# Optimization experiments

Hardware: AMD Instinct MI355X
Metric: run time of the kernel (lower is better)

## Reference

```python
import jax, jax.numpy as jnp
import numpy as np

# Config (matches init_kwargs)
B, C, H, W = 32, 128, 12, 1200   # z: (B, in_dim, H, W)
DIN = C * H                       # 1536
FIX = 768                         # get_multiple(DIN // 2, 6)
OV = 4                            # overlap
G = 6                             # num_vqs
D = OV * FIX // G                 # 512 per-group embedding size (all equal)
K = 1024                          # codebook_size
COMMIT = 0.25


def setup_inputs() -> dict:
    key = jax.random.key(0)
    k1, k2, k3, k4 = jax.random.split(key, 4)
    z = jax.random.normal(k1, (B, C, H, W), dtype=jnp.float32)
    w_down = jax.random.normal(k2, (FIX, DIN), dtype=jnp.float32) * 0.02
    w_up = jax.random.normal(k3, (DIN, FIX), dtype=jnp.float32) * 0.02
    embedding = jax.random.normal(k4, (G, D, K), dtype=jnp.float32)  # per-group (embedding_size, num_embedding)
    return {"z": z, "w_down": w_down, "w_up": w_up, "embedding": embedding}


def _quantize_group(zg, emb):
    # zg: (B, T, D), emb: (D, K)
    zf = zg.reshape(-1, D)
    # squared euclidean distance: |z|^2 - 2 z@E + |E|^2 -> (N, K)
    dist = (zf * zf).sum(1, keepdims=True) - 2.0 * (zf @ emb) + (emb * emb).sum(0, keepdims=True)
    idx = jnp.argmin(dist, axis=1)            # (N,)
    q = jnp.take(emb.T, idx, axis=0).reshape(zg.shape)
    # straight-through estimator (training mode)
    zq = zg + jax.lax.stop_gradient(q - zg)
    loss = COMMIT * jnp.mean((jax.lax.stop_gradient(zq) - zg) ** 2)
    return zq, loss


def reference(z, w_down, w_up, embedding):
    # pre_process: (B,C,H,W) -> permute(0,2,3,1) -> permute(0,2,3,1) -> (B, W, C*H)
    x = jnp.transpose(z, (0, 3, 1, 2)).reshape(B, W, DIN)  # (B, W, C, H) flattened
    x = x @ w_down.T                                       # proj_down -> (B, W, FIX)
    T = W // OV
    x = x.reshape(B, T, OV * FIX)                          # (B, T, 3072)
    # split into G contiguous groups of size D along last axis -> (G, B, T, D)
    xg = jnp.transpose(x.reshape(B, T, G, D), (2, 0, 1, 3))
    zq_g, losses = jax.vmap(_quantize_group)(xg, embedding)
    vq_loss = losses.sum() / G
    # concat groups back -> (B, T, G*D)
    zq = jnp.transpose(zq_g, (1, 2, 0, 3)).reshape(B, T, G * D)
    # post_process: un-overlap, proj_up, back to (B, C, H, W)
    zq = zq.reshape(B, W, FIX)
    zq = zq @ w_up.T                                       # (B, W, DIN)
    zq = zq.reshape(B, W, C, H)
    zq = jnp.transpose(zq, (0, 3, 1, 2))                   # (B, H, W, C)
    zq = jnp.transpose(zq, (0, 3, 1, 2))                   # dim==4 -> (B, C, H, W)
    return zq, vq_loss
```

## Files before the change

### kernel.cpp

```cpp
#include <hip/hip_runtime.h>

#define BB 32
#define CC 128
#define HH 12
#define WW 1200
#define DIN 1536
#define FIXD 768
#define OVL 4
#define GG 6
#define DD 512
#define KK 1024
#define TT 300
#define NV 9600
#define MROWS 38400

#define Y_OFF     0
#define ET_OFF    29491200
#define NORM_OFF  32636928
#define BEST_OFF  32643072
#define LOSS_OFF  32758272
#define ZN_OFF    32758336

#define BSWZ(c) ((c) + 4 * ((c) >> 5))

__global__ __launch_bounds__(256) void k_gemm_down(const float* __restrict__ z,
                                                   const float* __restrict__ w_down,
                                                   float* __restrict__ Y) {
    __shared__ float As[16][132];
    __shared__ float Bs[16][140];
    const int n0 = blockIdx.y * 128, f0 = blockIdx.x * 128;
    const int tid = threadIdx.x;
    const int arow = tid & 127;
    const int ak0 = tid >> 7;
    const int nA = n0 + arow;
    const int bA = nA / WW, wA = nA - bA * WW;
    const size_t zbase = (size_t)bA * (CC * HH * WW) + wA;
    const int bcol = tid >> 1, bq = tid & 1;
    const int bsc = BSWZ(bcol);
    const int trow = tid >> 4, tcol = tid & 15;
    const int bread = tcol * 8 + 4 * (tcol >> 2);
    float acc[8][8] = {};
    for (int kt = 0; kt < DIN; kt += 16) {
        #pragma unroll
        for (int i = 0; i < 8; i++) {
            const int kk = ak0 + i * 2;
            As[kk][arow] = z[zbase + (size_t)(kt + kk) * WW];
        }
        #pragma unroll
        for (int i = 0; i < 2; i++) {
            const int q = bq + i * 2;
            const float4 v = *(const float4*)&w_down[(size_t)(f0 + bcol) * DIN + kt + q * 4];
            Bs[q * 4 + 0][bsc] = v.x;
            Bs[q * 4 + 1][bsc] = v.y;
            Bs[q * 4 + 2][bsc] = v.z;
            Bs[q * 4 + 3][bsc] = v.w;
        }
        __syncthreads();
        #pragma unroll
        for (int k = 0; k < 16; k++) {
            float av[8], bv[8];
            *(float4*)&av[0] = *(const float4*)&As[k][trow * 8];
            *(float4*)&av[4] = *(const float4*)&As[k][trow * 8 + 4];
            *(float4*)&bv[0] = *(const float4*)&Bs[k][bread];
            *(float4*)&bv[4] = *(const float4*)&Bs[k][bread + 4];
            #pragma unroll
            for (int i = 0; i < 8; i++)
                #pragma unroll
                for (int j = 0; j < 8; j++)
                    acc[i][j] = fmaf(av[i], bv[j], acc[i][j]);
        }
        __syncthreads();
    }
    #pragma unroll
    for (int i = 0; i < 8; i++) {
        float4 o0, o1;
        o0.x = acc[i][0]; o0.y = acc[i][1]; o0.z = acc[i][2]; o0.w = acc[i][3];
        o1.x = acc[i][4]; o1.y = acc[i][5]; o1.z = acc[i][6]; o1.w = acc[i][7];
        float* yr = &Y[(size_t)(n0 + trow * 8 + i) * FIXD + f0 + tcol * 8];
        *(float4*)yr = o0;
        *(float4*)(yr + 4) = o1;
    }
}

__global__ __launch_bounds__(256) void k_transpose(const float* __restrict__ emb,
                                                   float* __restrict__ ET) {
    int i = blockIdx.x * 256 + threadIdx.x;
    if (i >= GG * KK * DD) return;
    int d = i & 511;
    int rem = i >> 9;
    int k = rem & 1023;
    int g = rem >> 10;
    ET[i] = emb[((g * DD + d) << 10) + k];
}

__global__ __launch_bounds__(64) void k_norms(const float* __restrict__ ET,
                                              float* __restrict__ norms) {
    const int code = blockIdx.x;
    const int lane = threadIdx.x;
    const float* row = ET + code * DD;
    double s = 0.0;
    #pragma unroll
    for (int r = 0; r < 8; r++) {
        float v = row[lane + r * 64];
        s += (double)v * (double)v;
    }
    #pragma unroll
    for (int off = 32; off; off >>= 1) s += __shfl_down(s, off);
    if (lane == 0) norms[code] = (float)s;
}

__global__ __launch_bounds__(256) void k_dist2(const float* __restrict__ Y,
                                               const float* __restrict__ ET,
                                               const float* __restrict__ norms,
                                               unsigned long long* __restrict__ best,
                                               float* __restrict__ znorm) {
    __shared__ float Zs[16][68];
    __shared__ float Es[16][140];
    __shared__ unsigned long long red[64][17];
    const int r = blockIdx.x;
    const int g = blockIdx.y;
    const int chunk = r / 48;
    const int wi = r - chunk * 48;
    const int vt = chunk * 6 + (wi % 6);
    const int ct = wi / 6;
    const int tid = threadIdx.x;
    const int rgrp = tid >> 4, cgrp = tid & 15;
    const int rbase = rgrp * 4;
    const int eread = cgrp * 8 + 4 * (cgrp >> 2);
    const int v0 = vt * 64, c0 = ct * 128;
    const float* ETg = ET + (size_t)g * KK * DD;

    const int zrow = tid >> 2, zq = tid & 3;
    const int vz = v0 + zrow;
    const int bz = vz / TT, tz = vz - bz * TT;

    float acc[4][8] = {};
    float zs = 0.0f;

    for (int kt = 0; kt < DD; kt += 16) {
        const int p0 = g * DD + kt;
        const int s = p0 / FIXD, f0 = p0 - s * FIXD;
        {
            const float4 v = *(const float4*)&Y[(bz * WW + tz * OVL + s) * FIXD + f0 + zq * 4];
            Zs[zq * 4 + 0][zrow] = v.x;
            Zs[zq * 4 + 1][zrow] = v.y;
            Zs[zq * 4 + 2][zrow] = v.z;
            Zs[zq * 4 + 3][zrow] = v.w;
            if (ct == 0) {
                zs = fmaf(v.x, v.x, zs);
                zs = fmaf(v.y, v.y, zs);
                zs = fmaf(v.z, v.z, zs);
                zs = fmaf(v.w, v.w, zs);
            }
        }
        #pragma unroll
        for (int i = 0; i < 2; i++) {
            int flat = tid + i * 256;
            int code = flat >> 2, q = flat & 3;
            const int sc = BSWZ(code);
            const float4 v = *(const float4*)&ETg[(size_t)(c0 + code) * DD + kt + q * 4];
            Es[q * 4 + 0][sc] = v.x;
            Es[q * 4 + 1][sc] = v.y;
            Es[q * 4 + 2][sc] = v.z;
            Es[q * 4 + 3][sc] = v.w;
        }
        __syncthreads();
        #pragma unroll
        for (int k = 0; k < 16; k++) {
            const float4 z4 = *(const float4*)&Zs[k][rbase];
            const float4 ea = *(const float4*)&Es[k][eread];
            const float4 eb = *(const float4*)&Es[k][eread + 4];
            const float zv[4] = {z4.x, z4.y, z4.z, z4.w};
            const float ev[8] = {ea.x, ea.y, ea.z, ea.w, eb.x, eb.y, eb.z, eb.w};
            #pragma unroll
            for (int i = 0; i < 4; i++)
                #pragma unroll
                for (int j = 0; j < 8; j++)
                    acc[i][j] = fmaf(zv[i], ev[j], acc[i][j]);
        }
        __syncthreads();
    }

    if (ct == 0) {
        float zsum = zs;
        zsum += __shfl_down(zsum, 2);
        zsum += __shfl_down(zsum, 1);
        if (zq == 0) znorm[g * NV + v0 + zrow] = zsum;
    }

    unsigned long long kbest[4];
    #pragma unroll
    for (int i = 0; i < 4; i++) kbest[i] = ~0ull;
    #pragma unroll
    for (int j = 0; j < 8; j++) {
        const int c = c0 + cgrp * 8 + j;
        const float nrm = norms[(g << 10) + c];
        #pragma unroll
        for (int i = 0; i < 4; i++) {
            float score = nrm - 2.0f * acc[i][j];
            unsigned u = __float_as_uint(score);
            u = (u & 0x80000000u) ? ~u : (u | 0x80000000u);
            unsigned long long key = ((unsigned long long)u << 32) | (unsigned)c;
            if (key < kbest[i]) kbest[i] = key;
        }
    }
    #pragma unroll
    for (int i = 0; i < 4; i++) red[rbase + i][cgrp] = kbest[i];
    __syncthreads();
    if (tid < 64) {
        unsigned long long b = red[tid][0];
        #pragma unroll
        for (int j = 1; j < 16; j++) {
            unsigned long long v = red[tid][j];
            if (v < b) b = v;
        }
        atomicMin(&best[g * NV + v0 + tid], b);
    }
}

__global__ __launch_bounds__(256) void k_sumloss(const unsigned long long* __restrict__ best,
                                                 const float* __restrict__ znorm,
                                                 float* __restrict__ lossAcc) {
    const int v = blockIdx.x * 256 + threadIdx.x;
    const unsigned long long key = best[v];
    const unsigned u = (unsigned)(key >> 32);
    const unsigned x = (u & 0x80000000u) ? (u & 0x7fffffffu) : ~u;
    float s = __uint_as_float(x) + znorm[v];
    __shared__ float red[256];
    red[threadIdx.x] = s;
    __syncthreads();
    for (int off = 128; off; off >>= 1) {
        if (threadIdx.x < off) red[threadIdx.x] += red[threadIdx.x + off];
        __syncthreads();
    }
    if (threadIdx.x == 0) atomicAdd(lossAcc, red[0]);
}

__constant__ int SEG_G[8]  = {0, 1, 1, 2, 3, 4, 4, 5};
__constant__ int SEG_D0[8] = {0, 0, 256, 0, 0, 0, 256, 0};
__constant__ int SEG_L[8]  = {512, 256, 256, 512, 512, 256, 256, 512};
__constant__ int SEG_F0[8] = {0, 512, 0, 256, 0, 512, 0, 256};

__global__ __launch_bounds__(256) void k_table(const float* __restrict__ ET,
                                               const float* __restrict__ w_up,
                                               float* __restrict__ Tab) {
    __shared__ float As[16][68];
    __shared__ float Bs[16][140];
    const int bm = blockIdx.x;
    const int bn = blockIdx.y;
    const int seg = blockIdx.z;
    const int g = SEG_G[seg], d0 = SEG_D0[seg], len = SEG_L[seg], fb = SEG_F0[seg];
    const int tid = threadIdx.x;
    const int k0 = bm * 64, dout0 = bn * 128;
    const int arow = tid >> 2, aq = tid & 3;
    const int rbase = (tid >> 4) << 2;
    const int cgrp = tid & 15;
    const int bread = cgrp * 8 + 4 * (cgrp >> 2);
    const float* ETg = ET + (size_t)(g << 10) * DD;
    float acc[4][8] = {};
    for (int kt = 0; kt < len; kt += 16) {
        {
            const float4 v = *(const float4*)&ETg[(size_t)(k0 + arow) * DD + d0 + kt + aq * 4];
            As[aq * 4 + 0][arow] = v.x;
            As[aq * 4 + 1][arow] = v.y;
            As[aq * 4 + 2][arow] = v.z;
            As[aq * 4 + 3][arow] = v.w;
        }
        #pragma unroll
        for (int i = 0; i < 2; i++) {
            int fl = tid + i * 256;
            int col = fl >> 2, q = fl & 3;
            const int sc = BSWZ(col);
            const float4 v = *(const float4*)&w_up[(size_t)(dout0 + col) * FIXD + fb + kt + q * 4];
            Bs[q * 4 + 0][sc] = v.x;
            Bs[q * 4 + 1][sc] = v.y;
            Bs[q * 4 + 2][sc] = v.z;
            Bs[q * 4 + 3][sc] = v.w;
        }
        __syncthreads();
        #pragma unroll
        for (int k = 0; k < 16; k++) {
            const float4 a  = *(const float4*)&As[k][rbase];
            const float4 ba = *(const float4*)&Bs[k][bread];
            const float4 bb = *(const float4*)&Bs[k][bread + 4];
            const float av[4] = {a.x, a.y, a.z, a.w};
            const float bv[8] = {ba.x, ba.y, ba.z, ba.w, bb.x, bb.y, bb.z, bb.w};
            #pragma unroll
            for (int i = 0; i < 4; i++)
                #pragma unroll
                for (int j = 0; j < 8; j++)
                    acc[i][j] = fmaf(av[i], bv[j], acc[i][j]);
        }
        __syncthreads();
    }
    #pragma unroll
    for (int i = 0; i < 4; i++) {
        float4 o0, o1;
        o0.x = acc[i][0]; o0.y = acc[i][1]; o0.z = acc[i][2]; o0.w = acc[i][3];
        o1.x = acc[i][4]; o1.y = acc[i][5]; o1.z = acc[i][6]; o1.w = acc[i][7];
        float* tr = &Tab[(size_t)((seg << 10) + k0 + rbase + i) * DIN + dout0 + cgrp * 8];
        *(float4*)tr = o0;
        *(float4*)(tr + 4) = o1;
    }
}

__global__ __launch_bounds__(256) void k_scatter(const float* __restrict__ Tab,
                                                 const unsigned long long* __restrict__ best,
                                                 float* __restrict__ out) {
    __shared__ float Ls[64][65];
    const int dt = blockIdx.x;
    const int wt = blockIdx.y;
    const int b  = blockIdx.z;
    const int dout0 = dt * 64, w0 = wt * 64;
    const int wlim = (WW - w0 < 64) ? (WW - w0) : 64;
    const int tid = threadIdx.x;
    const int wi = tid >> 2, q = tid & 3;

    if (wi < wlim) {
        const int w = w0 + wi;
        const int s = w & 3;
        const int t = w >> 2;
        const int gEt[4] = {0, 1, 3, 4};
        const int gOt[4] = {1, 2, 4, 5};
        int ce = (int)(unsigned)best[gEt[s] * NV + b * TT + t];
        int co = (int)(unsigned)best[gOt[s] * NV + b * TT + t];
        size_t rowE = (size_t)(((2 * s) << 10) + ce) * DIN;
        size_t rowO = (size_t)(((2 * s + 1) << 10) + co) * DIN;
        #pragma unroll
        for (int rep = 0; rep < 4; rep++) {
            const int doff = rep * 16 + q * 4;
            const float4 a = *(const float4*)&Tab[rowE + dout0 + doff];
            const float4 c = *(const float4*)&Tab[rowO + dout0 + doff];
            Ls[wi][doff + 0] = a.x + c.x;
            Ls[wi][doff + 1] = a.y + c.y;
            Ls[wi][doff + 2] = a.z + c.z;
            Ls[wi][doff + 3] = a.w + c.w;
        }
    }
    __syncthreads();
    const size_t obase = (size_t)b * (CC * HH * WW) + (size_t)dout0 * WW + w0;
    #pragma unroll
    for (int i = 0; i < 16; i++) {
        int flat = tid + i * 256;
        int dr = flat >> 6, wj = flat & 63;
        if (wj < wlim) out[obase + (size_t)dr * WW + wj] = Ls[wj][dr];
    }
}

__global__ void k_finish(const float* __restrict__ lossAcc, float* __restrict__ out) {
    if (threadIdx.x == 0)
        out[58982400] = lossAcc[0] * (0.25f / 29491200.0f);
}

extern "C" void kernel_launch(void* const* d_in, const int* in_sizes, int n_in,
                              void* d_out, int out_size, void* d_ws, size_t ws_size,
                              hipStream_t stream) {
    const float* z      = (const float*)d_in[0];
    const float* w_down = (const float*)d_in[1];
    const float* w_up   = (const float*)d_in[2];
    const float* emb    = (const float*)d_in[3];
    float* out = (float*)d_out;

    float* ws    = (float*)d_ws;
    float* Y     = ws + Y_OFF;
    float* Tab   = ws + Y_OFF;
    float* ET    = ws + ET_OFF;
    float* norms = ws + NORM_OFF;
    unsigned long long* best = (unsigned long long*)(ws + BEST_OFF);
    float* lossA = ws + LOSS_OFF;
    float* znorm = ws + ZN_OFF;

    hipMemsetAsync(best, 0xFF, (size_t)GG * NV * sizeof(unsigned long long), stream);
    hipMemsetAsync(lossA, 0, sizeof(float), stream);

    dim3 gdown(6, 300);
    k_gemm_down<<<gdown, 256, 0, stream>>>(z, w_down, Y);

    k_transpose<<<(GG * KK * DD + 255) / 256, 256, 0, stream>>>(emb, ET);
    k_norms<<<GG * KK, 64, 0, stream>>>(ET, norms);

    dim3 gdist(1200, GG);
    k_dist2<<<gdist, 256, 0, stream>>>(Y, ET, norms, best, znorm);

    k_sumloss<<<225, 256, 0, stream>>>(best, znorm, lossA);

    dim3 gtab(16, 12, 8);
    k_table<<<gtab, 256, 0, stream>>>(ET, w_up, Tab);

    dim3 gsc(24, 19, 32);
    k_scatter<<<gsc, 256, 0, stream>>>(Tab, best, out);

    k_finish<<<1, 64, 0, stream>>>(lossA, out);
}
```

Measured before the change: 2.091 ms.

## Use bf16 MFMA distance pass with candidate filtering and exact fp32 rescoring

Replaces the fp32 FMA distance/argmin kernel with a two-phase bf16 MFMA scheme. The first pass finds an approximate minimum per vector. The second recomputes the distances and collects every code within a Cauchy-Schwarz-based error margin. Those candidates are then rescored exactly in fp32, with a full fallback when more than 64 candidates qualify. This moves the dominant distance GEMM onto matrix cores, but it runs that GEMM twice and adds conversion kernels, atomics and rescoring work, so the argmin only matches the reference as long as the margin covers the bf16 error.

```diff
diff --git a/kernel.cpp b/kernel.cpp
--- a/kernel.cpp
+++ b/kernel.cpp
@@ -20,8 +20,27 @@
 #define BEST_OFF  32643072
 #define LOSS_OFF  32758272
 #define ZN_OFF    32758336
+#define UMIN_OFF  32815936
+#define CNT_OFF   32873536
+#define MAXN_OFF  32931136
+#define LIST_OFF  32931200
+#define YBF_OFF   36617600
+#define EBF_OFF   51363200
 
 #define BSWZ(c) ((c) + 4 * ((c) >> 5))
+
+typedef __attribute__((ext_vector_type(8))) short bf16x8;
+typedef __attribute__((ext_vector_type(4))) float f32x4;
+
+static __device__ inline unsigned short f2bf(float x) {
+    unsigned u = __float_as_uint(x);
+    unsigned r = (u + 0x7fffu + ((u >> 16) & 1u)) >> 16;
+    return (unsigned short)r;
+}
+static __device__ inline unsigned enc32(float s) {
+    unsigned u = __float_as_uint(s);
+    return (u & 0x80000000u) ? ~u : (u | 0x80000000u);
+}
 
 __global__ __launch_bounds__(256) void k_gemm_down(const float* __restrict__ z,
                                                    const float* __restrict__ w_down,
@@ -94,7 +113,8 @@
 }
 
 __global__ __launch_bounds__(64) void k_norms(const float* __restrict__ ET,
-                                              float* __restrict__ norms) {
+                                              float* __restrict__ norms,
+                                              unsigned* __restrict__ maxnU) {
     const int code = blockIdx.x;
     const int lane = threadIdx.x;
     const float* row = ET + code * DD;
@@ -106,116 +126,225 @@
     }
     #pragma unroll
     for (int off = 32; off; off >>= 1) s += __shfl_down(s, off);
-    if (lane == 0) norms[code] = (float)s;
-}
-
-__global__ __launch_bounds__(256) void k_dist2(const float* __restrict__ Y,
-                                               const float* __restrict__ ET,
+    if (lane == 0) {
+        const float nf = (float)s;
+        norms[code] = nf;
+        atomicMax(&maxnU[code >> 10], __float_as_uint(nf));
+    }
+}
+
+__global__ __launch_bounds__(256) void k_ysplit(const float* __restrict__ Y,
+                                                unsigned short* __restrict__ Ybf,
+                                                float* __restrict__ znorm) {
+    const int gv = blockIdx.x * 4 + (threadIdx.x >> 6);
+    const int lane = threadIdx.x & 63;
+    const int g = gv / NV, r = gv - g * NV;
+    const int b = r / TT, t = r - b * TT;
+    const int d0 = lane * 8;
+    const int p = g * DD + d0;
+    const int sg = p / FIXD, f = p - sg * FIXD;
+    const float* yb = &Y[(size_t)((b * WW + t * OVL + sg) * FIXD + f)];
+    const float4 y0 = *(const float4*)yb;
+    const float4 y1 = *(const float4*)(yb + 4);
+    unsigned short h[8];
+    h[0] = f2bf(y0.x); h[1] = f2bf(y0.y); h[2] = f2bf(y0.z); h[3] = f2bf(y0.w);
+    h[4] = f2bf(y1.x); h[5] = f2bf(y1.y); h[6] = f2bf(y1.z); h[7] = f2bf(y1.w);
+    *(uint4*)&Ybf[(size_t)gv * DD + d0] = *(uint4*)&h[0];
+    float s = 0.f;
+    s = fmaf(y0.x, y0.x, s); s = fmaf(y0.y, y0.y, s);
+    s = fmaf(y0.z, y0.z, s); s = fmaf(y0.w, y0.w, s);
+    s = fmaf(y1.x, y1.x, s); s = fmaf(y1.y, y1.y, s);
+    s = fmaf(y1.z, y1.z, s); s = fmaf(y1.w, y1.w, s);
+    #pragma unroll
+    for (int off = 32; off; off >>= 1) s += __shfl_down(s, off);
+    if (lane == 0) znorm[gv] = s;
+}
+
+__global__ __launch_bounds__(256) void k_esplit(const float* __restrict__ ET,
+                                                unsigned short* __restrict__ Ebf) {
+    const size_t i8 = ((size_t)blockIdx.x * 256 + threadIdx.x) * 8;
+    const float4 a = *(const float4*)&ET[i8];
+    const float4 b = *(const float4*)&ET[i8 + 4];
+    unsigned short h[8];
+    h[0] = f2bf(a.x); h[1] = f2bf(a.y); h[2] = f2bf(a.z); h[3] = f2bf(a.w);
+    h[4] = f2bf(b.x); h[5] = f2bf(b.y); h[6] = f2bf(b.z); h[7] = f2bf(b.w);
+    *(uint4*)&Ebf[i8] = *(uint4*)&h[0];
+}
+
+template<int PHASE>
+__global__ __launch_bounds__(256) void k_dist3(const unsigned short* __restrict__ Ybf,
+                                               const unsigned short* __restrict__ Ebf,
                                                const float* __restrict__ norms,
-                                               unsigned long long* __restrict__ best,
-                                               float* __restrict__ znorm) {
-    __shared__ float Zs[16][68];
-    __shared__ float Es[16][140];
-    __shared__ unsigned long long red[64][17];
-    const int r = blockIdx.x;
-    const int g = blockIdx.y;
-    const int chunk = r / 48;
-    const int wi = r - chunk * 48;
-    const int vt = chunk * 6 + (wi % 6);
-    const int ct = wi / 6;
+                                               const float* __restrict__ znorm,
+                                               const unsigned* __restrict__ maxnU,
+                                               unsigned* __restrict__ umin,
+                                               unsigned* __restrict__ cnt,
+                                               unsigned* __restrict__ list_) {
+    __shared__ unsigned short Ah[128][40], Bh[128][40];
+    __shared__ float a1s[128], margs[128];
+    const int vt = blockIdx.x;
+    const int ct = blockIdx.y;
+    const int g  = blockIdx.z;
+    const int v0 = vt * 128, c0 = ct * 128;
     const int tid = threadIdx.x;
-    const int rgrp = tid >> 4, cgrp = tid & 15;
-    const int rbase = rgrp * 4;
-    const int eread = cgrp * 8 + 4 * (cgrp >> 2);
-    const int v0 = vt * 64, c0 = ct * 128;
-    const float* ETg = ET + (size_t)g * KK * DD;
-
-    const int zrow = tid >> 2, zq = tid & 3;
-    const int vz = v0 + zrow;
-    const int bz = vz / TT, tz = vz - bz * TT;
-
-    float acc[4][8] = {};
-    float zs = 0.0f;
-
-    for (int kt = 0; kt < DD; kt += 16) {
-        const int p0 = g * DD + kt;
-        const int s = p0 / FIXD, f0 = p0 - s * FIXD;
+    const size_t ybase = ((size_t)g * NV + v0) * DD;
+    const size_t ebase = ((size_t)g * KK + c0) * DD;
+    const int srow = tid >> 1, sseg = (tid & 1) * 16;
+    const int wv = tid >> 6, lane = tid & 63;
+    const int wr = wv >> 1, wc = wv & 1;
+    const int m0 = wr * 64, n0 = wc * 64;
+    const int lr = lane & 15, lq = lane >> 4;
+
+    if (PHASE == 2 && tid < 128) {
+        const int gv = g * NV + v0 + tid;
+        const unsigned u = umin[gv];
+        const unsigned x = (u & 0x80000000u) ? (u & 0x7fffffffu) : ~u;
+        a1s[tid] = __uint_as_float(x);
+        margs[tid] = 0.032f * sqrtf(znorm[gv] * __uint_as_float(maxnU[g]));
+    }
+
+    f32x4 acc[4][4];
+    #pragma unroll
+    for (int i = 0; i < 4; i++)
+        #pragma unroll
+        for (int j = 0; j < 4; j++) acc[i][j] = (f32x4){0.f, 0.f, 0.f, 0.f};
+
+    for (int kt = 0; kt < DD; kt += 32) {
         {
-            const float4 v = *(const float4*)&Y[(bz * WW + tz * OVL + s) * FIXD + f0 + zq * 4];
-            Zs[zq * 4 + 0][zrow] = v.x;
-            Zs[zq * 4 + 1][zrow] = v.y;
-            Zs[zq * 4 + 2][zrow] = v.z;
-            Zs[zq * 4 + 3][zrow] = v.w;
-            if (ct == 0) {
-                zs = fmaf(v.x, v.x, zs);
-                zs = fmaf(v.y, v.y, zs);
-                zs = fmaf(v.z, v.z, zs);
-                zs = fmaf(v.w, v.w, zs);
+            const uint4 a0 = *(const uint4*)&Ybf[ybase + (size_t)srow * DD + kt + sseg];
+            const uint4 a1 = *(const uint4*)&Ybf[ybase + (size_t)srow * DD + kt + sseg + 8];
+            const uint4 b0 = *(const uint4*)&Ebf[ebase + (size_t)srow * DD + kt + sseg];
+            const uint4 b1 = *(const uint4*)&Ebf[ebase + (size_t)srow * DD + kt + sseg + 8];
+            *(uint4*)&Ah[srow][sseg]     = a0;
+            *(uint4*)&Ah[srow][sseg + 8] = a1;
+            *(uint4*)&Bh[srow][sseg]     = b0;
+            *(uint4*)&Bh[srow][sseg + 8] = b1;
+        }
+        __syncthreads();
+        bf16x8 ah[4], bh[4];
+        #pragma unroll
+        for (int i = 0; i < 4; i++) {
+            ah[i] = *(bf16x8*)&Ah[m0 + i * 16 + lr][lq * 8];
+            bh[i] = *(bf16x8*)&Bh[n0 + i * 16 + lr][lq * 8];
+        }
+        #pragma unroll
+        for (int i = 0; i < 4; i++)
+            #pragma unroll
+            for (int j = 0; j < 4; j++)
+                acc[i][j] = __builtin_amdgcn_mfma_f32_16x16x32_bf16(ah[i], bh[j], acc[i][j], 0, 0, 0);
+        __syncthreads();
+    }
+
+    float nrmj[4];
+    #pragma unroll
+    for (int j = 0; j < 4; j++) nrmj[j] = norms[(g << 10) + c0 + n0 + j * 16 + lr];
+
+    #pragma unroll
+    for (int i = 0; i < 4; i++) {
+        #pragma unroll
+        for (int rr = 0; rr < 4; rr++) {
+            const int row = m0 + i * 16 + lq * 4 + rr;
+            if (PHASE == 1) {
+                unsigned kb = 0xFFFFFFFFu;
+                #pragma unroll
+                for (int j = 0; j < 4; j++) {
+                    const unsigned u = enc32(nrmj[j] - 2.0f * acc[i][j][rr]);
+                    kb = (u < kb) ? u : kb;
+                }
+                #pragma unroll
+                for (int off = 1; off < 16; off <<= 1) {
+                    const unsigned o = __shfl_xor(kb, off);
+                    kb = (o < kb) ? o : kb;
+                }
+                if (lr == 0) atomicMin(&umin[g * NV + v0 + row], kb);
+            } else {
+                const float thr = a1s[row] + margs[row];
+                #pragma unroll
+                for (int j = 0; j < 4; j++) {
+                    const float sc = nrmj[j] - 2.0f * acc[i][j][rr];
+                    if (sc <= thr) {
+                        const int gv = g * NV + v0 + row;
+                        const unsigned idx = atomicAdd(&cnt[gv], 1u);
+                        if (idx < 64u)
+                            list_[(size_t)gv * 64 + idx] = (unsigned)(c0 + n0 + j * 16 + lr);
+                    }
+                }
             }
         }
-        #pragma unroll
-        for (int i = 0; i < 2; i++) {
-            int flat = tid + i * 256;
-            int code = flat >> 2, q = flat & 3;
-            const int sc = BSWZ(code);
-            const float4 v = *(const float4*)&ETg[(size_t)(c0 + code) * DD + kt + q * 4];
-            Es[q * 4 + 0][sc] = v.x;
-            Es[q * 4 + 1][sc] = v.y;
-            Es[q * 4 + 2][sc] = v.z;
-            Es[q * 4 + 3][sc] = v.w;
-        }
-        __syncthreads();
-        #pragma unroll
-        for (int k = 0; k < 16; k++) {
-            const float4 z4 = *(const float4*)&Zs[k][rbase];
-            const float4 ea = *(const float4*)&Es[k][eread];
-            const float4 eb = *(const float4*)&Es[k][eread + 4];
-            const float zv[4] = {z4.x, z4.y, z4.z, z4.w};
-            const float ev[8] = {ea.x, ea.y, ea.z, ea.w, eb.x, eb.y, eb.z, eb.w};
-            #pragma unroll
-            for (int i = 0; i < 4; i++)
-                #pragma unroll
-                for (int j = 0; j < 8; j++)
-                    acc[i][j] = fmaf(zv[i], ev[j], acc[i][j]);
-        }
-        __syncthreads();
-    }
-
-    if (ct == 0) {
-        float zsum = zs;
-        zsum += __shfl_down(zsum, 2);
-        zsum += __shfl_down(zsum, 1);
-        if (zq == 0) znorm[g * NV + v0 + zrow] = zsum;
-    }
-
-    unsigned long long kbest[4];
-    #pragma unroll
-    for (int i = 0; i < 4; i++) kbest[i] = ~0ull;
-    #pragma unroll
-    for (int j = 0; j < 8; j++) {
-        const int c = c0 + cgrp * 8 + j;
-        const float nrm = norms[(g << 10) + c];
-        #pragma unroll
-        for (int i = 0; i < 4; i++) {
-            float score = nrm - 2.0f * acc[i][j];
-            unsigned u = __float_as_uint(score);
-            u = (u & 0x80000000u) ? ~u : (u | 0x80000000u);
-            unsigned long long key = ((unsigned long long)u << 32) | (unsigned)c;
-            if (key < kbest[i]) kbest[i] = key;
-        }
-    }
-    #pragma unroll
-    for (int i = 0; i < 4; i++) red[rbase + i][cgrp] = kbest[i];
+    }
+}
+
+__global__ __launch_bounds__(64) void k_rescore(const float* __restrict__ Y,
+                                                const float* __restrict__ ET,
+                                                const float* __restrict__ norms,
+                                                const unsigned* __restrict__ cnt,
+                                                const unsigned* __restrict__ list_,
+                                                unsigned long long* __restrict__ best) {
+    const int gv = blockIdx.x;
+    const unsigned n = cnt[gv];
+    if (n == 0u || n > 64u) return;
+    const int lane = threadIdx.x;
+    const int g = gv / NV, r = gv - g * NV;
+    const int b = r / TT, t = r - b * TT;
+    unsigned long long key = ~0ull;
+    if (lane < (int)n) {
+        const unsigned c = list_[(size_t)gv * 64 + lane];
+        const float* erow = &ET[((size_t)((g << 10) + c)) * DD];
+        float s = 0.f;
+        for (int d4 = 0; d4 < 128; ++d4) {
+            const int p = g * DD + d4 * 4;
+            const int sg = p / FIXD, f = p - sg * FIXD;
+            const float4 yv = *(const float4*)&Y[(size_t)((b * WW + t * OVL + sg) * FIXD + f)];
+            const float4 ev = *(const float4*)&erow[d4 * 4];
+            s = fmaf(yv.x, ev.x, s); s = fmaf(yv.y, ev.y, s);
+            s = fmaf(yv.z, ev.z, s); s = fmaf(yv.w, ev.w, s);
+        }
+        const float sc = norms[(g << 10) + c] - 2.0f * s;
+        key = ((unsigned long long)enc32(sc) << 32) | c;
+    }
+    #pragma unroll
+    for (int off = 32; off; off >>= 1) {
+        const unsigned long long o = __shfl_down(key, off);
+        if (o < key) key = o;
+    }
+    if (lane == 0) best[gv] = key;
+}
+
+__global__ __launch_bounds__(256) void k_fallback(const float* __restrict__ Y,
+                                                  const float* __restrict__ ET,
+                                                  const float* __restrict__ norms,
+                                                  const unsigned* __restrict__ cnt,
+                                                  unsigned long long* __restrict__ best) {
+    const int gv = blockIdx.x;
+    if (cnt[gv] <= 64u) return;
+    __shared__ float Yv[512];
+    __shared__ unsigned long long red[256];
+    const int tid = threadIdx.x;
+    const int g = gv / NV, r = gv - g * NV;
+    const int b = r / TT, t = r - b * TT;
+    if (tid < 128) {
+        const int p = g * DD + tid * 4;
+        const int sg = p / FIXD, f = p - sg * FIXD;
+        *(float4*)&Yv[tid * 4] = *(const float4*)&Y[(size_t)((b * WW + t * OVL + sg) * FIXD + f)];
+    }
     __syncthreads();
-    if (tid < 64) {
-        unsigned long long b = red[tid][0];
-        #pragma unroll
-        for (int j = 1; j < 16; j++) {
-            unsigned long long v = red[tid][j];
-            if (v < b) b = v;
-        }
-        atomicMin(&best[g * NV + v0 + tid], b);
-    }
+    unsigned long long kb = ~0ull;
+    for (int cc = 0; cc < 4; ++cc) {
+        const int c = tid + cc * 256;
+        const float* erow = &ET[((size_t)((g << 10) + c)) * DD];
+        float s = 0.f;
+        for (int d = 0; d < 512; ++d) s = fmaf(Yv[d], erow[d], s);
+        const float sc = norms[(g << 10) + c] - 2.0f * s;
+        const unsigned long long key = ((unsigned long long)enc32(sc) << 32) | (unsigned)c;
+        if (key < kb) kb = key;
+    }
+    red[tid] = kb;
+    __syncthreads();
+    for (int off = 128; off; off >>= 1) {
+        if (tid < off) { if (red[tid + off] < red[tid]) red[tid] = red[tid + off]; }
+        __syncthreads();
+    }
+    if (tid == 0) best[gv] = red[0];
 }
 
 __global__ __launch_bounds__(256) void k_sumloss(const unsigned long long* __restrict__ best,
@@ -369,18 +498,34 @@
     unsigned long long* best = (unsigned long long*)(ws + BEST_OFF);
     float* lossA = ws + LOSS_OFF;
     float* znorm = ws + ZN_OFF;
+    unsigned* umin  = (unsigned*)(ws + UMIN_OFF);
+    unsigned* cnt   = (unsigned*)(ws + CNT_OFF);
+    unsigned* maxnU = (unsigned*)(ws + MAXN_OFF);
+    unsigned* list_ = (unsigned*)(ws + LIST_OFF);
+    unsigned short* Ybf = (unsigned short*)(ws + YBF_OFF);
+    unsigned short* Ebf = (unsigned short*)(ws + EBF_OFF);
 
     hipMemsetAsync(best, 0xFF, (size_t)GG * NV * sizeof(unsigned long long), stream);
+    hipMemsetAsync(umin, 0xFF, (size_t)GG * NV * sizeof(unsigned), stream);
+    hipMemsetAsync(cnt, 0, (size_t)GG * NV * sizeof(unsigned), stream);
+    hipMemsetAsync(maxnU, 0, 64, stream);
     hipMemsetAsync(lossA, 0, sizeof(float), stream);
 
     dim3 gdown(6, 300);
     k_gemm_down<<<gdown, 256, 0, stream>>>(z, w_down, Y);
 
     k_transpose<<<(GG * KK * DD + 255) / 256, 256, 0, stream>>>(emb, ET);
-    k_norms<<<GG * KK, 64, 0, stream>>>(ET, norms);
-
-    dim3 gdist(1200, GG);
-    k_dist2<<<gdist, 256, 0, stream>>>(Y, ET, norms, best, znorm);
+    k_norms<<<GG * KK, 64, 0, stream>>>(ET, norms, maxnU);
+
+    k_ysplit<<<GG * NV / 4, 256, 0, stream>>>(Y, Ybf, znorm);
+    k_esplit<<<GG * KK * DD / (256 * 8), 256, 0, stream>>>(ET, Ebf);
+
+    dim3 gdist(75, 8, GG);
+    k_dist3<1><<<gdist, 256, 0, stream>>>(Ybf, Ebf, norms, znorm, maxnU, umin, cnt, list_);
+    k_dist3<2><<<gdist, 256, 0, stream>>>(Ybf, Ebf, norms, znorm, maxnU, umin, cnt, list_);
+
+    k_rescore<<<GG * NV, 64, 0, stream>>>(Y, ET, norms, cnt, list_, best);
+    k_fallback<<<GG * NV, 256, 0, stream>>>(Y, ET, norms, cnt, best);
 
     k_sumloss<<<225, 256, 0, stream>>>(best, znorm, lossA);
 
```

New measurement: 2.001 ms. 4.3% less time.
